# Performance work log

Hardware: AMD Instinct MI355X
Metric: run time of the kernel (lower is better)

The kernel has to match this reference:

```python
import jax, jax.numpy as jnp
import numpy as np

DELTA_V = 0.5
DELTA_D = 1.5
LOSS_WEIGHT = 1.0


def setup_inputs() -> dict:
    key = jax.random.key(0)
    k1, k2, k3, k4 = jax.random.split(key, 4)
    B, D, H, W = 8, 4, 640, 640
    return {
        "emb": jax.random.normal(k1, (B, D, H, W), dtype=jnp.float32),
        "instance": jax.random.randint(k2, (B, H, W), 0, 33, dtype=jnp.int32),
        "kernel": jax.random.uniform(k3, (B, H, W), dtype=jnp.float32),
        "training_mask": jax.random.uniform(k4, (B, H, W), dtype=jnp.float32),
        "num_labels": 33,  # static: background label 0 + 32 instances, all present w.h.p.
    }


def _single(emb, instance, kernel, tmask, num_labels):
    # emb: [D,H,W]; instance: [H,W] int; kernel/tmask: [H,W] float
    D = emb.shape[0]
    tm = (tmask > 0.5).astype(instance.dtype)
    kn = (kernel > 0.5).astype(instance.dtype)
    inst2 = instance * tm                      # instance masked by training mask
    inst_k = (inst2 * kn).reshape(-1)          # kernel-restricted labels, [N]
    inst = inst2.reshape(-1)                   # [N]
    x = emb.reshape(D, -1).T                   # [N, D]
    ones = jnp.ones(x.shape[0], jnp.float32)

    # per-instance kernel means (scatter-mean), label 0 column forced to zero
    sums = jax.ops.segment_sum(x, inst_k, num_segments=num_labels)      # [K1, D]
    cnts = jax.ops.segment_sum(ones, inst_k, num_segments=num_labels)   # [K1]
    mean = sums / jnp.maximum(cnts, 1.0)[:, None]
    mean = mean.at[0].set(0.0)

    # aggregation term: per-pixel distance to its instance mean, segmented mean over labels 1..K
    diff = x - mean[inst]                                               # [N, D]
    dist = jnp.sqrt(jnp.sum(diff * diff, axis=1))
    val = jnp.log(jnp.maximum(dist - DELTA_V, 0.0) ** 2 + 1.0)
    cnt_i = jax.ops.segment_sum(ones, inst, num_segments=num_labels)
    agg = jax.ops.segment_sum(val, inst, num_segments=num_labels) / jnp.maximum(cnt_i, 1.0)
    l_agg = jnp.mean(agg[1:])

    # discrimination term: pairwise distances between instance means (exclude label 0 and diagonal)
    m = mean[1:]                                                        # [K, D]
    K = m.shape[0]
    pdiff = m[:, None, :] - m[None, :, :]
    pd = jnp.sqrt(jnp.sum(pdiff * pdiff, axis=-1) + jnp.eye(K))         # diag padded (masked below)
    vald = jnp.log(jnp.maximum(2.0 * DELTA_D - pd, 0.0) ** 2 + 1.0)
    off = 1.0 - jnp.eye(K)
    l_dis = jnp.sum(vald * off) / (K * (K - 1))

    # regularizer: mean over all num_labels columns; label-0 column contributes log(1)=0
    nrm1 = jnp.sqrt(jnp.sum(m * m, axis=1))
    l_reg = jnp.sum(jnp.log(nrm1 + 1.0)) / num_labels * 0.001

    return l_agg + l_dis + l_reg


def reference(emb, instance, kernel, training_mask, num_labels):
    f = lambda e, i, k, t: _single(e, i, k, t, num_labels)
    loss_batch = jax.vmap(f)(emb, instance, kernel, training_mask)
    return jnp.mean(LOSS_WEIGHT * loss_batch)
```

## Files before the change

kernel.cpp:

```cpp
#include <hip/hip_runtime.h>
#include <math.h>

#define HW    409600
#define HW4   102400
#define BATCH 8
#define NLAB  33
#define GXB   200
#define NREP  8
#define RS    201
#define WSB   208
#define LAB_OFF 8192
#define LAB_BYTES (4u * HW4 * BATCH)

__global__ void init_ws(float* ws) {
    int i = blockIdx.x * 256 + threadIdx.x;
    if (i < WSB * BATCH) ws[i] = 0.f;
}

__device__ __forceinline__ float getc(const float4& v, int e) {
    return (e == 0) ? v.x : (e == 1) ? v.y : (e == 2) ? v.z : v.w;
}
__device__ __forceinline__ int geti(const int4& v, int e) {
    return (e == 0) ? v.x : (e == 1) ? v.y : (e == 2) ? v.z : v.w;
}

__device__ __forceinline__ void acc1(int l, bool k,
                                     float x0, float x1, float x2, float x3,
                                     float* mb) {
    if (l) {
        float* bb = mb + l * 6;
        atomicAdd(bb + 5, 1.f);
        if (k) {
            atomicAdd(bb + 0, x0);
            atomicAdd(bb + 1, x1);
            atomicAdd(bb + 2, x2);
            atomicAdd(bb + 3, x3);
            atomicAdd(bb + 4, 1.f);
        }
    }
}

__global__ __launch_bounds__(256, 4) void pass1(const float* __restrict__ emb,
                                                const int*   __restrict__ inst,
                                                const float* __restrict__ kern,
                                                const float* __restrict__ tmask,
                                                float*       __restrict__ ws,
                                                unsigned*    __restrict__ labs) {
    __shared__ float bins[NREP][RS];
    const int t = threadIdx.x, bx = blockIdx.x, b = blockIdx.y;
    float* mb = bins[(t >> 3) & (NREP - 1)];
    for (int i = t; i < NREP * RS; i += 256) (&bins[0][0])[i] = 0.f;
    __syncthreads();

    const size_t  base  = (size_t)b * HW;
    const float4* emb4  = (const float4*)(emb + base * 4);
    const int4*   inst4 = (const int4*)(inst + base);
    const float4* kern4 = (const float4*)(kern + base);
    const float4* tm4   = (const float4*)(tmask + base);
    const int gA = bx * 512 + t, gB = gA + 256;

    int4   ivA = inst4[gA];          int4   ivB = inst4[gB];
    float4 tvA = tm4[gA];            float4 tvB = tm4[gB];
    float4 kvA = kern4[gA];          float4 kvB = kern4[gB];
    float4 x0A = emb4[gA];           float4 x0B = emb4[gB];
    float4 x1A = emb4[gA + HW4];     float4 x1B = emb4[gB + HW4];
    float4 x2A = emb4[gA + 2*HW4];   float4 x2B = emb4[gB + 2*HW4];
    float4 x3A = emb4[gA + 3*HW4];   float4 x3B = emb4[gB + 3*HW4];

    int lA0 = (tvA.x > 0.5f) ? ivA.x : 0;
    int lA1 = (tvA.y > 0.5f) ? ivA.y : 0;
    int lA2 = (tvA.z > 0.5f) ? ivA.z : 0;
    int lA3 = (tvA.w > 0.5f) ? ivA.w : 0;
    int lB0 = (tvB.x > 0.5f) ? ivB.x : 0;
    int lB1 = (tvB.y > 0.5f) ? ivB.y : 0;
    int lB2 = (tvB.z > 0.5f) ? ivB.z : 0;
    int lB3 = (tvB.w > 0.5f) ? ivB.w : 0;

    if (labs) {
        labs[(size_t)b * HW4 + gA] = (unsigned)lA0 | ((unsigned)lA1 << 8) |
                                     ((unsigned)lA2 << 16) | ((unsigned)lA3 << 24);
        labs[(size_t)b * HW4 + gB] = (unsigned)lB0 | ((unsigned)lB1 << 8) |
                                     ((unsigned)lB2 << 16) | ((unsigned)lB3 << 24);
    }

    acc1(lA0, kvA.x > 0.5f, x0A.x, x1A.x, x2A.x, x3A.x, mb);
    acc1(lA1, kvA.y > 0.5f, x0A.y, x1A.y, x2A.y, x3A.y, mb);
    acc1(lA2, kvA.z > 0.5f, x0A.z, x1A.z, x2A.z, x3A.z, mb);
    acc1(lA3, kvA.w > 0.5f, x0A.w, x1A.w, x2A.w, x3A.w, mb);
    acc1(lB0, kvB.x > 0.5f, x0B.x, x1B.x, x2B.x, x3B.x, mb);
    acc1(lB1, kvB.y > 0.5f, x0B.y, x1B.y, x2B.y, x3B.y, mb);
    acc1(lB2, kvB.z > 0.5f, x0B.z, x1B.z, x2B.z, x3B.z, mb);
    acc1(lB3, kvB.w > 0.5f, x0B.w, x1B.w, x2B.w, x3B.w, mb);
    __syncthreads();

    float* w = ws + b * WSB;
    for (int i = t; i < NLAB * 6; i += 256) {
        float v = 0.f;
        #pragma unroll
        for (int r = 0; r < NREP; ++r) v += bins[r][i];
        if (v != 0.f) {
            int lab = i / 6, f = i % 6;
            int dst = (f < 4) ? lab * 4 + f : ((f == 4) ? 132 + lab : 165 + lab);
            atomicAdd(w + dst, v);
        }
    }
}

template<bool USE_LABS>
__global__ __launch_bounds__(256, 4) void pass2(const float* __restrict__ emb,
                                                const int*   __restrict__ inst,
                                                const float* __restrict__ tmask,
                                                float*       __restrict__ ws,
                                                const unsigned* __restrict__ labs) {
    __shared__ float4 means4[NLAB];
    __shared__ float  invci[NLAB];
    __shared__ float  red[256];
    const int t = threadIdx.x, bx = blockIdx.x, b = blockIdx.y;
    float* w = ws + b * WSB;

    if (t < NLAB) {
        float inv = 1.f / fmaxf(w[132 + t], 1.f);
        float z = (t == 0) ? 0.f : 1.f;
        means4[t] = make_float4(z * w[t * 4 + 0] * inv, z * w[t * 4 + 1] * inv,
                                z * w[t * 4 + 2] * inv, z * w[t * 4 + 3] * inv);
        invci[t] = 1.f / fmaxf(w[165 + t], 1.f);
    }
    __syncthreads();

    const size_t  base = (size_t)b * HW;
    const float4* emb4 = (const float4*)(emb + base * 4);
    const int gA = bx * 512 + t, gB = gA + 256;

    unsigned pkA, pkB;
    if (USE_LABS) {
        pkA = labs[(size_t)b * HW4 + gA];
        pkB = labs[(size_t)b * HW4 + gB];
    } else {
        const int4*   inst4 = (const int4*)(inst + base);
        const float4* tm4   = (const float4*)(tmask + base);
        int4 ivA = inst4[gA], ivB = inst4[gB];
        float4 tvA = tm4[gA], tvB = tm4[gB];
        pkA = (unsigned)((tvA.x > 0.5f) ? ivA.x : 0)        |
              ((unsigned)((tvA.y > 0.5f) ? ivA.y : 0) << 8) |
              ((unsigned)((tvA.z > 0.5f) ? ivA.z : 0) << 16)|
              ((unsigned)((tvA.w > 0.5f) ? ivA.w : 0) << 24);
        pkB = (unsigned)((tvB.x > 0.5f) ? ivB.x : 0)        |
              ((unsigned)((tvB.y > 0.5f) ? ivB.y : 0) << 8) |
              ((unsigned)((tvB.z > 0.5f) ? ivB.z : 0) << 16)|
              ((unsigned)((tvB.w > 0.5f) ? ivB.w : 0) << 24);
    }

    float4 x0A = emb4[gA];           float4 x0B = emb4[gB];
    float4 x1A = emb4[gA + HW4];     float4 x1B = emb4[gB + HW4];
    float4 x2A = emb4[gA + 2*HW4];   float4 x2B = emb4[gB + 2*HW4];
    float4 x3A = emb4[gA + 3*HW4];   float4 x3B = emb4[gB + 3*HW4];

    float acc = 0.f;
    #pragma unroll
    for (int e = 0; e < 4; ++e) {
        int l = (pkA >> (8 * e)) & 255;
        if (l) {
            float4 m = means4[l];
            float d0 = getc(x0A, e) - m.x, d1 = getc(x1A, e) - m.y;
            float d2 = getc(x2A, e) - m.z, d3 = getc(x3A, e) - m.w;
            float dist = sqrtf(d0 * d0 + d1 * d1 + d2 * d2 + d3 * d3);
            float u = fmaxf(dist - 0.5f, 0.f);
            acc += __logf(u * u + 1.f) * invci[l];
        }
    }
    #pragma unroll
    for (int e = 0; e < 4; ++e) {
        int l = (pkB >> (8 * e)) & 255;
        if (l) {
            float4 m = means4[l];
            float d0 = getc(x0B, e) - m.x, d1 = getc(x1B, e) - m.y;
            float d2 = getc(x2B, e) - m.z, d3 = getc(x3B, e) - m.w;
            float dist = sqrtf(d0 * d0 + d1 * d1 + d2 * d2 + d3 * d3);
            float u = fmaxf(dist - 0.5f, 0.f);
            acc += __logf(u * u + 1.f) * invci[l];
        }
    }

    red[t] = acc;
    __syncthreads();
    for (int s = 128; s > 0; s >>= 1) {
        if (t < s) red[t] += red[t + s];
        __syncthreads();
    }
    if (t == 0) atomicAdd(w + 198, red[0]);
}

__global__ __launch_bounds__(256) void final_kernel(const float* __restrict__ ws,
                                                    float* __restrict__ out) {
    __shared__ float4 means4[NLAB];
    __shared__ float  red[256];
    int t = threadIdx.x;
    float total = 0.f;
    for (int b = 0; b < BATCH; ++b) {
        const float* w = ws + b * WSB;
        __syncthreads();
        if (t < NLAB) {
            float inv = 1.f / fmaxf(w[132 + t], 1.f);
            float z = (t == 0) ? 0.f : 1.f;
            means4[t] = make_float4(z * w[t * 4 + 0] * inv, z * w[t * 4 + 1] * inv,
                                    z * w[t * 4 + 2] * inv, z * w[t * 4 + 3] * inv);
        }
        __syncthreads();
        float part = 0.f;
        if (t == 0) part = w[198] * (1.f / 32.f);
        float disp = 0.f;
        for (int p = t; p < 1024; p += 256) {
            int i = p >> 5, j = p & 31;
            if (i != j) {
                float4 mi = means4[i + 1], mj = means4[j + 1];
                float d0 = mi.x - mj.x, d1 = mi.y - mj.y;
                float d2 = mi.z - mj.z, d3 = mi.w - mj.w;
                float pd = sqrtf(d0 * d0 + d1 * d1 + d2 * d2 + d3 * d3);
                float u = fmaxf(3.0f - pd, 0.f);
                disp += __logf(u * u + 1.f);
            }
        }
        disp *= 1.f / 992.f;
        float regp = 0.f;
        if (t >= 1 && t < NLAB) {
            float4 m = means4[t];
            float n2 = m.x * m.x + m.y * m.y + m.z * m.z + m.w * m.w;
            regp = __logf(sqrtf(n2) + 1.f) * (0.001f / 33.f);
        }
        red[t] = part + disp + regp;
        __syncthreads();
        for (int s = 128; s > 0; s >>= 1) {
            if (t < s) red[t] += red[t + s];
            __syncthreads();
        }
        if (t == 0) total += red[0];
    }
    if (t == 0) out[0] = total * (1.f / BATCH);
}

extern "C" void kernel_launch(void* const* d_in, const int* in_sizes, int n_in,
                              void* d_out, int out_size, void* d_ws, size_t ws_size,
                              hipStream_t stream) {
    const float* emb   = (const float*)d_in[0];
    const int*   inst  = (const int*)  d_in[1];
    const float* kern  = (const float*)d_in[2];
    const float* tmask = (const float*)d_in[3];
    float* ws  = (float*)d_ws;
    float* out = (float*)d_out;

    const bool use_labs = ws_size >= (size_t)LAB_OFF + LAB_BYTES;
    unsigned* labs = use_labs ? (unsigned*)((char*)d_ws + LAB_OFF) : nullptr;

    init_ws<<<dim3((WSB * BATCH + 255) / 256), 256, 0, stream>>>(ws);
    dim3 grid(GXB, BATCH);
    pass1<<<grid, 256, 0, stream>>>(emb, inst, kern, tmask, ws, labs);
    if (use_labs) pass2<true ><<<grid, 256, 0, stream>>>(emb, inst, tmask, ws, labs);
    else          pass2<false><<<grid, 256, 0, stream>>>(emb, inst, tmask, ws, nullptr);
    final_kernel<<<1, 256, 0, stream>>>(ws, out);
}
```

Baseline: 173.3 us.

## Halve per-thread work, double grid, wave-shuffle reductions, parallelize final over batch

Each thread in pass1 and pass2 now handles one float4 group instead of two, and the grid doubles to 400 blocks per batch with launch bounds raised to 8 blocks per CU. Global loads are issued before the shared-memory init and mean setup so they overlap. Block reductions now use wave shuffles instead of an LDS tree. The final kernel runs one block per batch element and accumulates into the output atomically, which init_ws zeroes. The aim is more occupancy and latency hiding on a memory-bound pass, at the cost of twice as many LDS bin flushes and global atomics per batch.

```diff
diff --git a/kernel.cpp b/kernel.cpp
--- a/kernel.cpp
+++ b/kernel.cpp
@@ -5,23 +5,27 @@
 #define HW4   102400
 #define BATCH 8
 #define NLAB  33
-#define GXB   200
+#define GXB   400
 #define NREP  8
 #define RS    201
 #define WSB   208
 #define LAB_OFF 8192
 #define LAB_BYTES (4u * HW4 * BATCH)
 
-__global__ void init_ws(float* ws) {
+__global__ void init_ws(float* ws, float* out) {
     int i = blockIdx.x * 256 + threadIdx.x;
     if (i < WSB * BATCH) ws[i] = 0.f;
+    if (i == 0) out[0] = 0.f;
 }
 
 __device__ __forceinline__ float getc(const float4& v, int e) {
     return (e == 0) ? v.x : (e == 1) ? v.y : (e == 2) ? v.z : v.w;
 }
-__device__ __forceinline__ int geti(const int4& v, int e) {
-    return (e == 0) ? v.x : (e == 1) ? v.y : (e == 2) ? v.z : v.w;
+
+__device__ __forceinline__ float wave_sum(float v) {
+    #pragma unroll
+    for (int o = 32; o > 0; o >>= 1) v += __shfl_xor(v, o);
+    return v;
 }
 
 __device__ __forceinline__ void acc1(int l, bool k,
@@ -40,7 +44,7 @@
     }
 }
 
-__global__ __launch_bounds__(256, 4) void pass1(const float* __restrict__ emb,
+__global__ __launch_bounds__(256, 8) void pass1(const float* __restrict__ emb,
                                                 const int*   __restrict__ inst,
                                                 const float* __restrict__ kern,
                                                 const float* __restrict__ tmask,
@@ -49,48 +53,38 @@
     __shared__ float bins[NREP][RS];
     const int t = threadIdx.x, bx = blockIdx.x, b = blockIdx.y;
     float* mb = bins[(t >> 3) & (NREP - 1)];
-    for (int i = t; i < NREP * RS; i += 256) (&bins[0][0])[i] = 0.f;
-    __syncthreads();
 
     const size_t  base  = (size_t)b * HW;
     const float4* emb4  = (const float4*)(emb + base * 4);
     const int4*   inst4 = (const int4*)(inst + base);
     const float4* kern4 = (const float4*)(kern + base);
     const float4* tm4   = (const float4*)(tmask + base);
-    const int gA = bx * 512 + t, gB = gA + 256;
-
-    int4   ivA = inst4[gA];          int4   ivB = inst4[gB];
-    float4 tvA = tm4[gA];            float4 tvB = tm4[gB];
-    float4 kvA = kern4[gA];          float4 kvB = kern4[gB];
-    float4 x0A = emb4[gA];           float4 x0B = emb4[gB];
-    float4 x1A = emb4[gA + HW4];     float4 x1B = emb4[gB + HW4];
-    float4 x2A = emb4[gA + 2*HW4];   float4 x2B = emb4[gB + 2*HW4];
-    float4 x3A = emb4[gA + 3*HW4];   float4 x3B = emb4[gB + 3*HW4];
-
-    int lA0 = (tvA.x > 0.5f) ? ivA.x : 0;
-    int lA1 = (tvA.y > 0.5f) ? ivA.y : 0;
-    int lA2 = (tvA.z > 0.5f) ? ivA.z : 0;
-    int lA3 = (tvA.w > 0.5f) ? ivA.w : 0;
-    int lB0 = (tvB.x > 0.5f) ? ivB.x : 0;
-    int lB1 = (tvB.y > 0.5f) ? ivB.y : 0;
-    int lB2 = (tvB.z > 0.5f) ? ivB.z : 0;
-    int lB3 = (tvB.w > 0.5f) ? ivB.w : 0;
-
-    if (labs) {
-        labs[(size_t)b * HW4 + gA] = (unsigned)lA0 | ((unsigned)lA1 << 8) |
-                                     ((unsigned)lA2 << 16) | ((unsigned)lA3 << 24);
-        labs[(size_t)b * HW4 + gB] = (unsigned)lB0 | ((unsigned)lB1 << 8) |
-                                     ((unsigned)lB2 << 16) | ((unsigned)lB3 << 24);
-    }
-
-    acc1(lA0, kvA.x > 0.5f, x0A.x, x1A.x, x2A.x, x3A.x, mb);
-    acc1(lA1, kvA.y > 0.5f, x0A.y, x1A.y, x2A.y, x3A.y, mb);
-    acc1(lA2, kvA.z > 0.5f, x0A.z, x1A.z, x2A.z, x3A.z, mb);
-    acc1(lA3, kvA.w > 0.5f, x0A.w, x1A.w, x2A.w, x3A.w, mb);
-    acc1(lB0, kvB.x > 0.5f, x0B.x, x1B.x, x2B.x, x3B.x, mb);
-    acc1(lB1, kvB.y > 0.5f, x0B.y, x1B.y, x2B.y, x3B.y, mb);
-    acc1(lB2, kvB.z > 0.5f, x0B.z, x1B.z, x2B.z, x3B.z, mb);
-    acc1(lB3, kvB.w > 0.5f, x0B.w, x1B.w, x2B.w, x3B.w, mb);
+    const int g = bx * 256 + t;
+
+    int4   iv = inst4[g];
+    float4 tv = tm4[g];
+    float4 kv = kern4[g];
+    float4 x0 = emb4[g];
+    float4 x1 = emb4[g + HW4];
+    float4 x2 = emb4[g + 2 * HW4];
+    float4 x3 = emb4[g + 3 * HW4];
+
+    for (int i = t; i < NREP * RS; i += 256) (&bins[0][0])[i] = 0.f;
+    __syncthreads();
+
+    int l0 = (tv.x > 0.5f) ? iv.x : 0;
+    int l1 = (tv.y > 0.5f) ? iv.y : 0;
+    int l2 = (tv.z > 0.5f) ? iv.z : 0;
+    int l3 = (tv.w > 0.5f) ? iv.w : 0;
+
+    if (labs)
+        labs[(size_t)b * HW4 + g] = (unsigned)l0 | ((unsigned)l1 << 8) |
+                                    ((unsigned)l2 << 16) | ((unsigned)l3 << 24);
+
+    acc1(l0, kv.x > 0.5f, x0.x, x1.x, x2.x, x3.x, mb);
+    acc1(l1, kv.y > 0.5f, x0.y, x1.y, x2.y, x3.y, mb);
+    acc1(l2, kv.z > 0.5f, x0.z, x1.z, x2.z, x3.z, mb);
+    acc1(l3, kv.w > 0.5f, x0.w, x1.w, x2.w, x3.w, mb);
     __syncthreads();
 
     float* w = ws + b * WSB;
@@ -107,16 +101,38 @@
 }
 
 template<bool USE_LABS>
-__global__ __launch_bounds__(256, 4) void pass2(const float* __restrict__ emb,
+__global__ __launch_bounds__(256, 8) void pass2(const float* __restrict__ emb,
                                                 const int*   __restrict__ inst,
                                                 const float* __restrict__ tmask,
                                                 float*       __restrict__ ws,
                                                 const unsigned* __restrict__ labs) {
     __shared__ float4 means4[NLAB];
     __shared__ float  invci[NLAB];
-    __shared__ float  red[256];
+    __shared__ float  red[4];
     const int t = threadIdx.x, bx = blockIdx.x, b = blockIdx.y;
     float* w = ws + b * WSB;
+
+    const size_t  base = (size_t)b * HW;
+    const float4* emb4 = (const float4*)(emb + base * 4);
+    const int g = bx * 256 + t;
+
+    unsigned pk;
+    if (USE_LABS) {
+        pk = labs[(size_t)b * HW4 + g];
+    } else {
+        const int4*   inst4 = (const int4*)(inst + base);
+        const float4* tm4   = (const float4*)(tmask + base);
+        int4 iv = inst4[g];
+        float4 tv = tm4[g];
+        pk = (unsigned)((tv.x > 0.5f) ? iv.x : 0)        |
+             ((unsigned)((tv.y > 0.5f) ? iv.y : 0) << 8) |
+             ((unsigned)((tv.z > 0.5f) ? iv.z : 0) << 16)|
+             ((unsigned)((tv.w > 0.5f) ? iv.w : 0) << 24);
+    }
+    float4 x0 = emb4[g];
+    float4 x1 = emb4[g + HW4];
+    float4 x2 = emb4[g + 2 * HW4];
+    float4 x3 = emb4[g + 3 * HW4];
 
     if (t < NLAB) {
         float inv = 1.f / fmaxf(w[132 + t], 1.f);
@@ -127,115 +143,68 @@
     }
     __syncthreads();
 
-    const size_t  base = (size_t)b * HW;
-    const float4* emb4 = (const float4*)(emb + base * 4);
-    const int gA = bx * 512 + t, gB = gA + 256;
-
-    unsigned pkA, pkB;
-    if (USE_LABS) {
-        pkA = labs[(size_t)b * HW4 + gA];
-        pkB = labs[(size_t)b * HW4 + gB];
-    } else {
-        const int4*   inst4 = (const int4*)(inst + base);
-        const float4* tm4   = (const float4*)(tmask + base);
-        int4 ivA = inst4[gA], ivB = inst4[gB];
-        float4 tvA = tm4[gA], tvB = tm4[gB];
-        pkA = (unsigned)((tvA.x > 0.5f) ? ivA.x : 0)        |
-              ((unsigned)((tvA.y > 0.5f) ? ivA.y : 0) << 8) |
-              ((unsigned)((tvA.z > 0.5f) ? ivA.z : 0) << 16)|
-              ((unsigned)((tvA.w > 0.5f) ? ivA.w : 0) << 24);
-        pkB = (unsigned)((tvB.x > 0.5f) ? ivB.x : 0)        |
-              ((unsigned)((tvB.y > 0.5f) ? ivB.y : 0) << 8) |
-              ((unsigned)((tvB.z > 0.5f) ? ivB.z : 0) << 16)|
-              ((unsigned)((tvB.w > 0.5f) ? ivB.w : 0) << 24);
-    }
-
-    float4 x0A = emb4[gA];           float4 x0B = emb4[gB];
-    float4 x1A = emb4[gA + HW4];     float4 x1B = emb4[gB + HW4];
-    float4 x2A = emb4[gA + 2*HW4];   float4 x2B = emb4[gB + 2*HW4];
-    float4 x3A = emb4[gA + 3*HW4];   float4 x3B = emb4[gB + 3*HW4];
-
     float acc = 0.f;
     #pragma unroll
     for (int e = 0; e < 4; ++e) {
-        int l = (pkA >> (8 * e)) & 255;
+        int l = (pk >> (8 * e)) & 255;
         if (l) {
             float4 m = means4[l];
-            float d0 = getc(x0A, e) - m.x, d1 = getc(x1A, e) - m.y;
-            float d2 = getc(x2A, e) - m.z, d3 = getc(x3A, e) - m.w;
+            float d0 = getc(x0, e) - m.x, d1 = getc(x1, e) - m.y;
+            float d2 = getc(x2, e) - m.z, d3 = getc(x3, e) - m.w;
             float dist = sqrtf(d0 * d0 + d1 * d1 + d2 * d2 + d3 * d3);
             float u = fmaxf(dist - 0.5f, 0.f);
             acc += __logf(u * u + 1.f) * invci[l];
         }
     }
-    #pragma unroll
-    for (int e = 0; e < 4; ++e) {
-        int l = (pkB >> (8 * e)) & 255;
-        if (l) {
-            float4 m = means4[l];
-            float d0 = getc(x0B, e) - m.x, d1 = getc(x1B, e) - m.y;
-            float d2 = getc(x2B, e) - m.z, d3 = getc(x3B, e) - m.w;
-            float dist = sqrtf(d0 * d0 + d1 * d1 + d2 * d2 + d3 * d3);
-            float u = fmaxf(dist - 0.5f, 0.f);
-            acc += __logf(u * u + 1.f) * invci[l];
-        }
-    }
-
-    red[t] = acc;
-    __syncthreads();
-    for (int s = 128; s > 0; s >>= 1) {
-        if (t < s) red[t] += red[t + s];
-        __syncthreads();
-    }
-    if (t == 0) atomicAdd(w + 198, red[0]);
+
+    acc = wave_sum(acc);
+    if ((t & 63) == 0) red[t >> 6] = acc;
+    __syncthreads();
+    if (t == 0) atomicAdd(w + 198, red[0] + red[1] + red[2] + red[3]);
 }
 
 __global__ __launch_bounds__(256) void final_kernel(const float* __restrict__ ws,
                                                     float* __restrict__ out) {
     __shared__ float4 means4[NLAB];
-    __shared__ float  red[256];
-    int t = threadIdx.x;
-    float total = 0.f;
-    for (int b = 0; b < BATCH; ++b) {
-        const float* w = ws + b * WSB;
-        __syncthreads();
-        if (t < NLAB) {
-            float inv = 1.f / fmaxf(w[132 + t], 1.f);
-            float z = (t == 0) ? 0.f : 1.f;
-            means4[t] = make_float4(z * w[t * 4 + 0] * inv, z * w[t * 4 + 1] * inv,
-                                    z * w[t * 4 + 2] * inv, z * w[t * 4 + 3] * inv);
-        }
-        __syncthreads();
-        float part = 0.f;
-        if (t == 0) part = w[198] * (1.f / 32.f);
-        float disp = 0.f;
-        for (int p = t; p < 1024; p += 256) {
-            int i = p >> 5, j = p & 31;
-            if (i != j) {
-                float4 mi = means4[i + 1], mj = means4[j + 1];
-                float d0 = mi.x - mj.x, d1 = mi.y - mj.y;
-                float d2 = mi.z - mj.z, d3 = mi.w - mj.w;
-                float pd = sqrtf(d0 * d0 + d1 * d1 + d2 * d2 + d3 * d3);
-                float u = fmaxf(3.0f - pd, 0.f);
-                disp += __logf(u * u + 1.f);
-            }
-        }
-        disp *= 1.f / 992.f;
-        float regp = 0.f;
-        if (t >= 1 && t < NLAB) {
-            float4 m = means4[t];
-            float n2 = m.x * m.x + m.y * m.y + m.z * m.z + m.w * m.w;
-            regp = __logf(sqrtf(n2) + 1.f) * (0.001f / 33.f);
-        }
-        red[t] = part + disp + regp;
-        __syncthreads();
-        for (int s = 128; s > 0; s >>= 1) {
-            if (t < s) red[t] += red[t + s];
-            __syncthreads();
-        }
-        if (t == 0) total += red[0];
-    }
-    if (t == 0) out[0] = total * (1.f / BATCH);
+    __shared__ float  red[4];
+    const int t = threadIdx.x, b = blockIdx.x;
+    const float* w = ws + b * WSB;
+
+    if (t < NLAB) {
+        float inv = 1.f / fmaxf(w[132 + t], 1.f);
+        float z = (t == 0) ? 0.f : 1.f;
+        means4[t] = make_float4(z * w[t * 4 + 0] * inv, z * w[t * 4 + 1] * inv,
+                                z * w[t * 4 + 2] * inv, z * w[t * 4 + 3] * inv);
+    }
+    __syncthreads();
+
+    float part = 0.f;
+    if (t == 0) part = w[198] * (1.f / 32.f);
+    float disp = 0.f;
+    for (int p = t; p < 1024; p += 256) {
+        int i = p >> 5, j = p & 31;
+        if (i != j) {
+            float4 mi = means4[i + 1], mj = means4[j + 1];
+            float d0 = mi.x - mj.x, d1 = mi.y - mj.y;
+            float d2 = mi.z - mj.z, d3 = mi.w - mj.w;
+            float pd = sqrtf(d0 * d0 + d1 * d1 + d2 * d2 + d3 * d3);
+            float u = fmaxf(3.0f - pd, 0.f);
+            disp += __logf(u * u + 1.f);
+        }
+    }
+    disp *= 1.f / 992.f;
+    float regp = 0.f;
+    if (t >= 1 && t < NLAB) {
+        float4 m = means4[t];
+        float n2 = m.x * m.x + m.y * m.y + m.z * m.z + m.w * m.w;
+        regp = __logf(sqrtf(n2) + 1.f) * (0.001f / 33.f);
+    }
+
+    float v = wave_sum(part + disp + regp);
+    if ((t & 63) == 0) red[t >> 6] = v;
+    __syncthreads();
+    if (t == 0)
+        atomicAdd(out, (red[0] + red[1] + red[2] + red[3]) * (1.f / BATCH));
 }
 
 extern "C" void kernel_launch(void* const* d_in, const int* in_sizes, int n_in,
@@ -251,10 +220,10 @@
     const bool use_labs = ws_size >= (size_t)LAB_OFF + LAB_BYTES;
     unsigned* labs = use_labs ? (unsigned*)((char*)d_ws + LAB_OFF) : nullptr;
 
-    init_ws<<<dim3((WSB * BATCH + 255) / 256), 256, 0, stream>>>(ws);
+    init_ws<<<dim3((WSB * BATCH + 255) / 256), 256, 0, stream>>>(ws, out);
     dim3 grid(GXB, BATCH);
     pass1<<<grid, 256, 0, stream>>>(emb, inst, kern, tmask, ws, labs);
     if (use_labs) pass2<true ><<<grid, 256, 0, stream>>>(emb, inst, tmask, ws, labs);
     else          pass2<false><<<grid, 256, 0, stream>>>(emb, inst, tmask, ws, nullptr);
-    final_kernel<<<1, 256, 0, stream>>>(ws, out);
-}
+    final_kernel<<<BATCH, 256, 0, stream>>>(ws, out);
+}
```

New measurement: 189.6 us. 1.09x slower.
